# Optimization experiments

Measured on AMD Instinct MI355X. Metric: run time of the kernel, lower is better.

Reference implementation:

```python
import jax, jax.numpy as jnp
import numpy as np

N_NODES = 100000
N_EDGES = 3200000
N_GRAPHS = 2048
D_IN = 128
D_H = 128
D_OUT = 2
BN_EPS = 1e-5


def setup_inputs() -> dict:
    key = jax.random.key(0)
    ks = jax.random.split(key, 24)
    x = jax.random.normal(ks[0], (N_NODES, D_IN), dtype=jnp.float32)
    edge_index = jax.random.randint(ks[1], (2, N_EDGES), 0, N_NODES, dtype=jnp.int64)
    batch = jnp.sort(jax.random.randint(ks[2], (N_NODES,), 0, N_GRAPHS, dtype=jnp.int64))

    def lin(k, din, dout):
        return jax.random.normal(k, (din, dout), dtype=jnp.float32) / np.sqrt(din)

    inp = {
        'x': x, 'edge_index': edge_index, 'batch': batch,
        'W1': lin(ks[3], D_IN, D_H), 'b1': jnp.zeros((D_H,), jnp.float32),
        'W2': lin(ks[4], D_H, D_H), 'b2': jnp.zeros((D_H,), jnp.float32),
        'W3': lin(ks[5], D_H, D_H), 'b3': jnp.zeros((D_H,), jnp.float32),
    }
    for i, kk in zip((1, 2, 3), (ks[6], ks[7], ks[8])):
        inp[f'bn{i}_g'] = 1.0 + 0.1 * jax.random.normal(jax.random.fold_in(kk, 0), (D_H,), jnp.float32)
        inp[f'bn{i}_b'] = 0.1 * jax.random.normal(jax.random.fold_in(kk, 1), (D_H,), jnp.float32)
        inp[f'bn{i}_m'] = 0.1 * jax.random.normal(jax.random.fold_in(kk, 2), (D_H,), jnp.float32)
        inp[f'bn{i}_v'] = 0.5 + jax.random.uniform(jax.random.fold_in(kk, 3), (D_H,), jnp.float32)
    inp['fc1_W'] = lin(ks[9], D_H, D_H)
    inp['fc1_b'] = jnp.zeros((D_H,), jnp.float32)
    inp['fc2_W'] = lin(ks[10], D_H, D_OUT)
    inp['fc2_b'] = jnp.zeros((D_OUT,), jnp.float32)
    return inp


def _gcn_conv(x, W, b, src, dst, dinv):
    # h = X W, then out[dst] += (dinv[src]*dinv[dst]) * h[src]  (self-loops already in src/dst)
    h = x @ W
    norm = dinv[src] * dinv[dst]  # [E+N]
    msg = h[src] * norm[:, None]  # [E+N, D]
    out = jax.ops.segment_sum(msg, dst, num_segments=N_NODES)
    return out + b


def _bn_eval(x, g, b, m, v):
    return (x - m) * (g * jax.lax.rsqrt(v + BN_EPS)) + b


def reference(x, edge_index, batch, W1, b1, W2, b2, W3, b3,
              bn1_g, bn1_b, bn1_m, bn1_v, bn2_g, bn2_b, bn2_m, bn2_v,
              bn3_g, bn3_b, bn3_m, bn3_v, fc1_W, fc1_b, fc2_W, fc2_b):
    loops = jnp.arange(N_NODES, dtype=edge_index.dtype)
    src = jnp.concatenate([edge_index[0], loops])
    dst = jnp.concatenate([edge_index[1], loops])
    deg = jax.ops.segment_sum(jnp.ones_like(dst, dtype=x.dtype), dst, num_segments=N_NODES)
    dinv = jnp.where(deg > 0, jax.lax.rsqrt(jnp.maximum(deg, 1.0)), 0.0)

    h = jax.nn.relu(_bn_eval(_gcn_conv(x, W1, b1, src, dst, dinv), bn1_g, bn1_b, bn1_m, bn1_v))
    h = jax.nn.relu(_bn_eval(_gcn_conv(h, W2, b2, src, dst, dinv), bn2_g, bn2_b, bn2_m, bn2_v))
    h = jax.nn.relu(_bn_eval(_gcn_conv(h, W3, b3, src, dst, dinv), bn3_g, bn3_b, bn3_m, bn3_v))

    # global mean pool over graphs
    sums = jax.ops.segment_sum(h, batch, num_segments=N_GRAPHS)
    cnts = jax.ops.segment_sum(jnp.ones((N_NODES,), h.dtype), batch, num_segments=N_GRAPHS)
    pooled = sums / jnp.maximum(cnts, 1.0)[:, None]  # [G, D_H]

    z = jax.nn.relu(pooled @ fc1_W + fc1_b)
    logits = z @ fc2_W + fc2_b
    return jax.nn.log_softmax(logits, axis=1)
```

## Files before the change

kernel.cpp:

```cpp
#include <hip/hip_runtime.h>
#include <stdint.h>

#define NN 100000
#define NE 3200000
#define NG 2048
#define DH 128

#define NBUK 196
#define BSH 9
#define BMASK 511
#define BUKCAP 18200
#define EPT 16
#define EPW 4096

typedef __attribute__((ext_vector_type(8))) short v8s;
typedef __attribute__((ext_vector_type(4))) float v4f;
typedef __attribute__((ext_vector_type(2))) float f2;

__device__ __forceinline__ float bf2f(unsigned short u) {
  union { unsigned int i; float f; } v; v.i = ((unsigned int)u) << 16; return v.f;
}
__device__ __forceinline__ unsigned short f2bf(float f) {
  union { float f; unsigned int i; } v; v.f = f;
  unsigned int i = v.i;
  unsigned int r = (i + 0x7FFFu + ((i >> 16) & 1u)) >> 16;
  return (unsigned short)r;
}
__device__ __forceinline__ int eload(const void* p, long long i, int is64) {
  return is64 ? (int)((const long long*)p)[i] : ((const int*)p)[i];
}
__device__ __forceinline__ float pload(const void* p, int i, int isbf) {
  return isbf ? bf2f(((const unsigned short*)p)[i]) : ((const float*)p)[i];
}
__device__ __forceinline__ void upadd2(unsigned int w, f2& acc) {
  union { unsigned int u; float f; } a, b;
  a.u = w << 16; b.u = w & 0xffff0000u;
  f2 u; u.x = a.f; u.y = b.f;
  acc += u;
}

constexpr size_t al(size_t x) { return (x + 255) & ~size_t(255); }
constexpr size_t OFF_FLAGS = 0;
constexpr size_t OFF_DINV  = 256;
constexpr size_t OFF_ROWP  = al(OFF_DINV + 4ull * NN);
constexpr size_t OFF_GSTART= al(OFF_ROWP + 4ull * (NN + 1));
constexpr size_t OFF_BCUR  = al(OFF_GSTART + 4ull * (NG + 1));
constexpr size_t OFF_WT    = al(OFF_BCUR + 1024);
constexpr size_t OFF_FC1W  = al(OFF_WT + 2ull * 3 * 16384);
constexpr size_t OFF_FC2W  = al(OFF_FC1W + 4ull * 16384);
constexpr size_t OFF_PVEC  = al(OFF_FC2W + 4ull * 256);
constexpr size_t OFF_AC    = al(OFF_PVEC + 4ull * 17 * 128);
constexpr size_t OFF_COL   = al(OFF_AC + 4ull * 768);
constexpr size_t OFF_H     = al(OFF_COL + 4ull * NE);
constexpr size_t OFF_Y     = al(OFF_H + 2ull * NN * 128);
constexpr size_t WS_NEED   = OFF_Y + 2ull * NN * 128;
constexpr size_t OFF_REC   = OFF_H;


__global__ __launch_bounds__(256) void probe_k(const void* edge, const void* batch,
                                               const void* x, int* flags, int* bcur) {
  __shared__ int cnt_e, cnt_b, cnt_f;
  int t = threadIdx.x;
  bcur[t] = 0;
  if (t == 0) { cnt_e = 0; cnt_b = 0; cnt_f = 0; }
  __syncthreads();
  int le = 0, lb = 0, lf = 0;
  for (int i = t; i < 512; i += 256) {
    uint2 p = ((const uint2*)edge)[i + 64];
    if (p.y != 0) le++;
  }
  for (int i = t; i < 512; i += 256) {
    uint2 p = ((const uint2*)batch)[50000 - 512 + i];
    if (p.y != 0) lb++;
  }
  for (int i = t; i < 4096; i += 256) {
    unsigned short u = ((const unsigned short*)x)[i];
    int e = (u >> 7) & 0xFF;
    if (e >= 0x90) lf++;
  }
  atomicAdd(&cnt_e, le); atomicAdd(&cnt_b, lb); atomicAdd(&cnt_f, lf);
  __syncthreads();
  if (t == 0) {
    flags[0] = (cnt_e == 0);
    flags[1] = (cnt_b == 0);
    flags[2] = (cnt_f < 16);
    flags[3] = 1;
  }
}

struct Ptrs { const void* p[22]; };

__global__ __launch_bounds__(256) void norm_param_k(Ptrs ptrs, const int* flags,
    unsigned short* Wt, float* fc1W, float* fc2W, float* pvec) {
  int isbf = flags[2];
  int idx = blockIdx.x * 256 + threadIdx.x;
  if (idx < 3 * 16384) {
    int l = idx / 16384, rem = idx % 16384;
    int c = rem >> 7, k = rem & 127;
    const void* W = ptrs.p[2 * l];
    Wt[l * 16384 + c * DH + k] = f2bf(pload(W, k * DH + c, isbf));
  } else if (idx < 4 * 16384) {
    int jj = idx - 3 * 16384;
    fc1W[jj] = pload(ptrs.p[18], jj, isbf);
  } else if (idx < 4 * 16384 + 256) {
    int jj = idx - 4 * 16384;
    fc2W[jj] = pload(ptrs.p[20], jj, isbf);
  } else if (idx < 4 * 16384 + 256 + 17 * 128) {
    int jj = idx - (4 * 16384 + 256);
    int slot = jj >> 7, e = jj & 127;
    int pi = (slot < 3) ? (1 + 2 * slot) : (slot < 15) ? (slot + 3) : (slot == 15 ? 19 : 21);
    if (slot == 16 && e >= 2) return;
    pvec[slot * 128 + e] = pload(ptrs.p[pi], e, isbf);
  }
}

__global__ __launch_bounds__(256) void prep_k(const float* pvec, float* AC) {
  int idx = blockIdx.x * 256 + threadIdx.x;
  if (idx >= 384) return;
  int l = idx >> 7, d = idx & 127;
  float b  = pvec[l * 128 + d];
  float g  = pvec[(3 + 4 * l) * 128 + d];
  float bb = pvec[(4 + 4 * l) * 128 + d];
  float m  = pvec[(5 + 4 * l) * 128 + d];
  float v  = pvec[(6 + 4 * l) * 128 + d];
  float s = g * rsqrtf(v + 1e-5f);
  AC[l * 256 + d] = s;
  AC[l * 256 + 128 + d] = (b - m) * s + bb;
}

__global__ __launch_bounds__(256) void partition_k(const void* edge, const int* flags,
    int* bcur, unsigned long long* recs) {
  __shared__ int lhist[NBUK];
  __shared__ int lbase[NBUK];
  __shared__ int lrank[NBUK];
  int t = threadIdx.x;
  for (int b = t; b < NBUK; b += 256) { lhist[b] = 0; lrank[b] = 0; }
  __syncthreads();
  long long e0 = (long long)blockIdx.x * EPW;
  int f = flags[0];
  int sv[EPT], dv[EPT];
  #pragma unroll
  for (int k = 0; k < EPT; ++k) {
    long long e = e0 + k * 256 + t;
    int s = 0, d = -1;
    if (e < NE) {
      s = eload(edge, e, f);
      d = eload(edge, NE + e, f);
      if ((unsigned)s >= NN || (unsigned)d >= NN) d = -1;
    }
    sv[k] = s; dv[k] = d;
    if (d >= 0) atomicAdd(&lhist[d >> BSH], 1);
  }
  __syncthreads();
  for (int b = t; b < NBUK; b += 256)
    lbase[b] = atomicAdd(&bcur[b], lhist[b]);
  __syncthreads();
  #pragma unroll
  for (int k = 0; k < EPT; ++k) {
    int d = dv[k];
    if (d >= 0) {
      int b = d >> BSH;
      int r = atomicAdd(&lrank[b], 1);
      int pos = lbase[b] + r;
      if (pos < BUKCAP)
        recs[(size_t)b * BUKCAP + pos] =
            ((unsigned long long)(unsigned)d << 32) | (unsigned)sv[k];
    }
  }
}

__global__ __launch_bounds__(256) void csr_build_k(const unsigned long long* recs,
    const int* bcur, int* rowp, int* colv, float* dinv) {
  __shared__ int lh[512];
  __shared__ int lcur[512];
  __shared__ int lts[256];
  __shared__ int lstart;
  int b = blockIdx.x, t = threadIdx.x;
  {
    int v = (t < b && t < NBUK) ? min(bcur[t], BUKCAP) : 0;
    lts[t] = v; __syncthreads();
    for (int off = 128; off > 0; off >>= 1) {
      if (t < off) lts[t] += lts[t + off];
      __syncthreads();
    }
    if (t == 0) lstart = lts[0];
  }
  for (int i = t; i < 512; i += 256) lh[i] = 0;
  __syncthreads();
  int cnt = min(bcur[b], BUKCAP);
  const unsigned long long* rb = recs + (size_t)b * BUKCAP;
  for (int i = t; i < cnt; i += 256)
    atomicAdd(&lh[(int)(rb[i] >> 32) & BMASK], 1);
  __syncthreads();
  int e0 = lh[2 * t], e1 = lh[2 * t + 1];
  lts[t] = e0 + e1; __syncthreads();
  for (int off = 1; off < 256; off <<= 1) {
    int x = (t >= off) ? lts[t - off] : 0;
    __syncthreads();
    lts[t] += x;
    __syncthreads();
  }
  int pre = lts[t] - (e0 + e1);
  int base = b << BSH;
  int n0 = base + 2 * t, n1 = base + 2 * t + 1;
  int r0 = lstart + pre, r1 = lstart + pre + e0;
  if (n0 < NN) { rowp[n0] = r0; dinv[n0] = rsqrtf((float)(e0 + 1)); }
  if (n1 < NN) { rowp[n1] = r1; dinv[n1] = rsqrtf((float)(e1 + 1)); }
  lcur[2 * t] = r0; lcur[2 * t + 1] = r1;
  if (b == NBUK - 1 && t == 255) rowp[NN] = lstart + lts[255];
  __syncthreads();
  for (int i = t; i < cnt; i += 256) {
    unsigned long long rec = rb[i];
    int d = (int)(rec >> 32);
    int s = (int)(rec & 0xffffffffu);
    int p = atomicAdd(&lcur[d & BMASK], 1);
    colv[p] = s;
  }
}

__global__ __launch_bounds__(256) void gbound_k(const void* batch, const int* flags,
                                                int* gstart) {
  int i = blockIdx.x * 256 + threadIdx.x;
  if (i >= NN) return;
  int f = flags[1];
  int b = eload(batch, i, f);
  if ((unsigned)b >= NG) b = NG - 1;
  int bp = -1;
  if (i > 0) {
    bp = eload(batch, i - 1, f);
    if ((unsigned)bp >= NG) bp = NG - 1;
  }
  for (int g = bp + 1; g <= b; ++g) gstart[g] = i;
  if (i == NN - 1) {
    for (int g = b + 1; g <= NG; ++g) gstart[g] = NN;
  }
}

__global__ __launch_bounds__(256) void gemm_k(const void* A, const int* flagp,
    const unsigned short* Wt, const float* dinv, unsigned short* H) {
  const int wave = threadIdx.x >> 6;
  const int lane = threadIdx.x & 63;
  const int rowbase = blockIdx.x * 64 + wave * 16;
  const int r = lane & 15;
  const int g = lane >> 4;
  const int isb = flagp[0];
  int arow = rowbase + r;
  int arowc = (arow < NN) ? arow : 0;

  v8s a[4];
  if (isb) {
    const uint4* Ab = (const uint4*)A;
    #pragma unroll
    for (int ks = 0; ks < 4; ++ks) {
      union { uint4 u; v8s v; } t;
      t.u = Ab[(arowc * DH + ks * 32 + g * 8) >> 3];
      a[ks] = t.v;
    }
  } else {
    const float4* Af = (const float4*)A;
    #pragma unroll
    for (int ks = 0; ks < 4; ++ks) {
      int bi = (arowc * DH + ks * 32 + g * 8) >> 2;
      float4 f0 = Af[bi], f1 = Af[bi + 1];
      v8s t;
      t[0]=(short)f2bf(f0.x); t[1]=(short)f2bf(f0.y); t[2]=(short)f2bf(f0.z); t[3]=(short)f2bf(f0.w);
      t[4]=(short)f2bf(f1.x); t[5]=(short)f2bf(f1.y); t[6]=(short)f2bf(f1.z); t[7]=(short)f2bf(f1.w);
      a[ks] = t;
    }
  }
  int orow0 = rowbase + g * 4;
  float dv[4];
  #pragma unroll
  for (int j = 0; j < 4; ++j) {
    int orow = orow0 + j;
    dv[j] = dinv[(orow < NN) ? orow : 0];
  }
  const uint4* Wb = (const uint4*)Wt;
  #pragma unroll
  for (int ct = 0; ct < 8; ++ct) {
    v4f acc = {0.f, 0.f, 0.f, 0.f};
    #pragma unroll
    for (int ks = 0; ks < 4; ++ks) {
      union { uint4 u; v8s v; } t;
      t.u = Wb[((ct * 16 + r) * DH + ks * 32 + g * 8) >> 3];
      acc = __builtin_amdgcn_mfma_f32_16x16x32_bf16(a[ks], t.v, acc, 0, 0, 0);
    }
    #pragma unroll
    for (int j = 0; j < 4; ++j) {
      int orow = orow0 + j;
      if (orow < NN) H[orow * DH + ct * 16 + r] = f2bf(acc[j] * dv[j]);
    }
  }
}

__global__ __launch_bounds__(256) void agg_k(const unsigned short* H, const int* rowp,
    const int* colv, const float* dinv, const float* Avec, const float* Cvec,
    unsigned short* Y) {
  int n = blockIdx.x * 4 + (threadIdx.x >> 6);
  if (n >= NN) return;
  int lane = threadIdx.x & 63;
  int q = lane >> 4;
  int c16 = lane & 15;
  const uint4* Hc = (const uint4*)H + c16;
  f2 a01 = {0.f, 0.f}, a23 = {0.f, 0.f}, a45 = {0.f, 0.f}, a67 = {0.f, 0.f};
  int beg = rowp[n], end = rowp[n + 1];
  int j = beg;
  #define ACC4(v) do { upadd2((v).x, a01); upadd2((v).y, a23); \
                       upadd2((v).z, a45); upadd2((v).w, a67); } while (0)
  for (; j + 16 <= end; j += 16) {
    int s0 = colv[j + q];
    int s1 = colv[j + 4 + q];
    int s2 = colv[j + 8 + q];
    int s3 = colv[j + 12 + q];
    uint4 v0 = Hc[s0 * 16];
    uint4 v1 = Hc[s1 * 16];
    uint4 v2 = Hc[s2 * 16];
    uint4 v3 = Hc[s3 * 16];
    ACC4(v0); ACC4(v1); ACC4(v2); ACC4(v3);
  }
  for (; j + 4 <= end; j += 4) {
    int s0 = colv[j + q];
    uint4 v0 = Hc[s0 * 16];
    ACC4(v0);
  }
  if (j + q < end) {
    uint4 v0 = Hc[colv[j + q] * 16];
    ACC4(v0);
  }
  #undef ACC4
  #pragma unroll
  for (int m = 16; m <= 32; m <<= 1) {
    a01.x += __shfl_xor(a01.x, m); a01.y += __shfl_xor(a01.y, m);
    a23.x += __shfl_xor(a23.x, m); a23.y += __shfl_xor(a23.y, m);
    a45.x += __shfl_xor(a45.x, m); a45.y += __shfl_xor(a45.y, m);
    a67.x += __shfl_xor(a67.x, m); a67.y += __shfl_xor(a67.y, m);
  }
  if (q == 0) {
    uint4 sv = Hc[n * 16];
    upadd2(sv.x, a01); upadd2(sv.y, a23);
    upadd2(sv.z, a45); upadd2(sv.w, a67);
    float dvn = dinv[n];
    int f0 = c16 * 8;
    float y0 = fmaxf(a01.x * dvn * Avec[f0+0] + Cvec[f0+0], 0.f);
    float y1 = fmaxf(a01.y * dvn * Avec[f0+1] + Cvec[f0+1], 0.f);
    float y2 = fmaxf(a23.x * dvn * Avec[f0+2] + Cvec[f0+2], 0.f);
    float y3 = fmaxf(a23.y * dvn * Avec[f0+3] + Cvec[f0+3], 0.f);
    float y4 = fmaxf(a45.x * dvn * Avec[f0+4] + Cvec[f0+4], 0.f);
    float y5 = fmaxf(a45.y * dvn * Avec[f0+5] + Cvec[f0+5], 0.f);
    float y6 = fmaxf(a67.x * dvn * Avec[f0+6] + Cvec[f0+6], 0.f);
    float y7 = fmaxf(a67.y * dvn * Avec[f0+7] + Cvec[f0+7], 0.f);
    uint4 o;
    o.x = (unsigned int)f2bf(y0) | ((unsigned int)f2bf(y1) << 16);
    o.y = (unsigned int)f2bf(y2) | ((unsigned int)f2bf(y3) << 16);
    o.z = (unsigned int)f2bf(y4) | ((unsigned int)f2bf(y5) << 16);
    o.w = (unsigned int)f2bf(y6) | ((unsigned int)f2bf(y7) << 16);
    ((uint4*)Y)[n * 16 + c16] = o;
  }
}

__global__ __launch_bounds__(256) void pool_k(const unsigned short* Y, const int* gstart,
                                              float* pooled) {
  int g = blockIdx.x * 4 + (threadIdx.x >> 6);
  if (g >= NG) return;
  int lane = threadIdx.x & 63;
  const unsigned int* Yu = (const unsigned int*)Y;
  int beg = gstart[g], end = gstart[g + 1];
  int cnt = end - beg;
  float a0 = 0.f, a1 = 0.f;
  for (int i = beg; i < end; ++i) {
    unsigned int v = Yu[i * 64 + lane];
    a0 += bf2f((unsigned short)v); a1 += bf2f((unsigned short)(v >> 16));
  }
  float inv = 1.f / fmaxf((float)cnt, 1.f);
  pooled[g * DH + lane * 2]     = a0 * inv;
  pooled[g * DH + lane * 2 + 1] = a1 * inv;
}

__global__ __launch_bounds__(256) void fc1_k(const float* pooled, const float* fc1W,
                                             const float* pvec, float* Z) {
  int idx = blockIdx.x * 256 + threadIdx.x;
  int g = idx >> 7, c = idx & 127;
  if (g >= NG) return;
  float acc = 0.f;
  const float* pr = pooled + g * DH;
  #pragma unroll 8
  for (int k = 0; k < DH; ++k) acc += pr[k] * fc1W[k * DH + c];
  acc += pvec[15 * 128 + c];
  Z[g * DH + c] = fmaxf(acc, 0.f);
}

__global__ __launch_bounds__(256) void fc2_k(const float* Z, const float* fc2W,
                                             const float* pvec, float* out) {
  int g = blockIdx.x * 256 + threadIdx.x;
  if (g >= NG) return;
  float l0 = pvec[16 * 128 + 0], l1 = pvec[16 * 128 + 1];
  const float* zr = Z + g * DH;
  #pragma unroll 8
  for (int k = 0; k < DH; ++k) { float z = zr[k]; l0 += z * fc2W[k * 2]; l1 += z * fc2W[k * 2 + 1]; }
  float m = fmaxf(l0, l1);
  float lse = m + logf(expf(l0 - m) + expf(l1 - m));
  out[g * 2]     = l0 - lse;
  out[g * 2 + 1] = l1 - lse;
}

extern "C" void kernel_launch(void* const* d_in, const int* in_sizes, int n_in,
                              void* d_out, int out_size, void* d_ws, size_t ws_size,
                              hipStream_t stream) {
  char* ws = (char*)d_ws;
  int*   flags  = (int*)(ws + OFF_FLAGS);
  float* dinvp  = (float*)(ws + OFF_DINV);
  int*   rowp   = (int*)(ws + OFF_ROWP);
  int*   gstart = (int*)(ws + OFF_GSTART);
  int*   bcur   = (int*)(ws + OFF_BCUR);
  unsigned short* Wt  = (unsigned short*)(ws + OFF_WT);
  float* fc1W   = (float*)(ws + OFF_FC1W);
  float* fc2W   = (float*)(ws + OFF_FC2W);
  float* pvec   = (float*)(ws + OFF_PVEC);
  float* AC     = (float*)(ws + OFF_AC);
  int*   colv   = (int*)(ws + OFF_COL);
  unsigned short* Hbuf = (unsigned short*)(ws + OFF_H);
  unsigned short* Ybuf = (unsigned short*)(ws + OFF_Y);
  unsigned long long* recs = (unsigned long long*)(ws + OFF_REC);
  float* pooled = (float*)(ws + OFF_COL);
  float* Z      = (float*)(ws + OFF_COL + 4ull * NG * DH);

  const void* x     = d_in[0];
  const void* edge  = d_in[1];
  const void* batch = d_in[2];

  probe_k<<<1, 256, 0, stream>>>(edge, batch, x, flags, bcur);

  Ptrs P;
  for (int i = 0; i < 22; ++i) P.p[i] = d_in[3 + i];
  norm_param_k<<<266, 256, 0, stream>>>(P, flags, Wt, fc1W, fc2W, pvec);
  prep_k<<<2, 256, 0, stream>>>(pvec, AC);

  partition_k<<<(NE + EPW - 1) / EPW, 256, 0, stream>>>(edge, flags, bcur, recs);
  gbound_k<<<(NN + 255) / 256, 256, 0, stream>>>(batch, flags, gstart);
  csr_build_k<<<NBUK, 256, 0, stream>>>(recs, bcur, rowp, colv, dinvp);

  const int GB = (NN + 63) / 64;
  gemm_k<<<GB, 256, 0, stream>>>(x, flags + 2, Wt, dinvp, Hbuf);
  agg_k<<<NN / 4, 256, 0, stream>>>(Hbuf, rowp, colv, dinvp, AC, AC + 128, Ybuf);
  gemm_k<<<GB, 256, 0, stream>>>(Ybuf, flags + 3, Wt + 16384, dinvp, Hbuf);
  agg_k<<<NN / 4, 256, 0, stream>>>(Hbuf, rowp, colv, dinvp, AC + 256, AC + 384, Ybuf);
  gemm_k<<<GB, 256, 0, stream>>>(Ybuf, flags + 3, Wt + 32768, dinvp, Hbuf);
  agg_k<<<NN / 4, 256, 0, stream>>>(Hbuf, rowp, colv, dinvp, AC + 512, AC + 640, Ybuf);

  pool_k<<<NG / 4, 256, 0, stream>>>(Ybuf, gstart, pooled);
  fc1_k<<<(NG * DH) / 256, 256, 0, stream>>>(pooled, fc1W, pvec, Z);
  fc2_k<<<(NG + 255) / 256, 256, 0, stream>>>(Z, fc2W, pvec, (float*)d_out);
}
```

Baseline: 564.6 us.

## Fuse aggregation with next-layer GEMM via LDS staging

Adds a kernel that aggregates 64 node rows per block, applies the BN and ReLU epilogue, stages the bf16 result in shared memory, and then runs the next layer's MFMA GEMM on it. The intermediate Y is no longer written to and read back from global memory between layers 1-2 and 2-3, and two launches are removed. The gather loop is also deepened to 32 edges per iteration. The trade-off is less parallelism: each wave now handles 16 rows in sequence instead of one row per wave, with only 1563 blocks, which can hurt latency hiding for the irregular gathers.

Measured after the change: 609.7 us. +8.0%, slower.

```diff
diff --git a/kernel.cpp b/kernel.cpp
--- a/kernel.cpp
+++ b/kernel.cpp
@@ -13,6 +13,8 @@
 #define EPT 16
 #define EPW 4096
 
+#define LROW 136
+
 typedef __attribute__((ext_vector_type(8))) short v8s;
 typedef __attribute__((ext_vector_type(4))) float v4f;
 typedef __attribute__((ext_vector_type(2))) float f2;
@@ -37,6 +39,40 @@
   a.u = w << 16; b.u = w & 0xffff0000u;
   f2 u; u.x = a.f; u.y = b.f;
   acc += u;
+}
+#define ACC4(v) do { upadd2((v).x, a01); upadd2((v).y, a23); \
+                     upadd2((v).z, a45); upadd2((v).w, a67); } while (0)
+
+__device__ __forceinline__ void gather_row(const uint4* Hc, const int* colv,
+    int beg, int end, int q, f2& a01, f2& a23, f2& a45, f2& a67) {
+  int j = beg;
+  for (; j + 32 <= end; j += 32) {
+    int s0 = colv[j + q],      s1 = colv[j + 4 + q];
+    int s2 = colv[j + 8 + q],  s3 = colv[j + 12 + q];
+    int s4 = colv[j + 16 + q], s5 = colv[j + 20 + q];
+    int s6 = colv[j + 24 + q], s7 = colv[j + 28 + q];
+    uint4 v0 = Hc[s0 * 16]; uint4 v1 = Hc[s1 * 16];
+    uint4 v2 = Hc[s2 * 16]; uint4 v3 = Hc[s3 * 16];
+    uint4 v4 = Hc[s4 * 16]; uint4 v5 = Hc[s5 * 16];
+    uint4 v6 = Hc[s6 * 16]; uint4 v7 = Hc[s7 * 16];
+    ACC4(v0); ACC4(v1); ACC4(v2); ACC4(v3);
+    ACC4(v4); ACC4(v5); ACC4(v6); ACC4(v7);
+  }
+  for (; j + 16 <= end; j += 16) {
+    int s0 = colv[j + q],     s1 = colv[j + 4 + q];
+    int s2 = colv[j + 8 + q], s3 = colv[j + 12 + q];
+    uint4 v0 = Hc[s0 * 16]; uint4 v1 = Hc[s1 * 16];
+    uint4 v2 = Hc[s2 * 16]; uint4 v3 = Hc[s3 * 16];
+    ACC4(v0); ACC4(v1); ACC4(v2); ACC4(v3);
+  }
+  for (; j + 4 <= end; j += 4) {
+    uint4 v0 = Hc[colv[j + q] * 16];
+    ACC4(v0);
+  }
+  if (j + q < end) {
+    uint4 v0 = Hc[colv[j + q] * 16];
+    ACC4(v0);
+  }
 }
 
 constexpr size_t al(size_t x) { return (x + 255) & ~size_t(255); }
@@ -293,6 +329,89 @@
   }
 }
 
+__global__ __launch_bounds__(256) void aggemm_k(const unsigned short* H,
+    const int* rowp, const int* colv, const float* dinv,
+    const float* Avec, const float* Cvec, const unsigned short* Wt,
+    unsigned short* Hout) {
+  __shared__ unsigned short Ylds[64 * LROW];
+  int wid = threadIdx.x >> 6, lane = threadIdx.x & 63;
+  int q = lane >> 4, c16 = lane & 15;
+  int base = blockIdx.x * 64;
+  const uint4* Hc = (const uint4*)H + c16;
+  for (int i = 0; i < 16; ++i) {
+    int row = wid * 16 + i;
+    int n = base + row;
+    if (n < NN) {
+      f2 a01 = {0.f,0.f}, a23 = {0.f,0.f}, a45 = {0.f,0.f}, a67 = {0.f,0.f};
+      int beg = rowp[n], end = rowp[n + 1];
+      gather_row(Hc, colv, beg, end, q, a01, a23, a45, a67);
+      #pragma unroll
+      for (int m = 16; m <= 32; m <<= 1) {
+        a01.x += __shfl_xor(a01.x, m); a01.y += __shfl_xor(a01.y, m);
+        a23.x += __shfl_xor(a23.x, m); a23.y += __shfl_xor(a23.y, m);
+        a45.x += __shfl_xor(a45.x, m); a45.y += __shfl_xor(a45.y, m);
+        a67.x += __shfl_xor(a67.x, m); a67.y += __shfl_xor(a67.y, m);
+      }
+      if (q == 0) {
+        uint4 sv = Hc[n * 16];
+        upadd2(sv.x, a01); upadd2(sv.y, a23);
+        upadd2(sv.z, a45); upadd2(sv.w, a67);
+        float dvn = dinv[n];
+        int f0 = c16 * 8;
+        float y0 = fmaxf(a01.x * dvn * Avec[f0+0] + Cvec[f0+0], 0.f);
+        float y1 = fmaxf(a01.y * dvn * Avec[f0+1] + Cvec[f0+1], 0.f);
+        float y2 = fmaxf(a23.x * dvn * Avec[f0+2] + Cvec[f0+2], 0.f);
+        float y3 = fmaxf(a23.y * dvn * Avec[f0+3] + Cvec[f0+3], 0.f);
+        float y4 = fmaxf(a45.x * dvn * Avec[f0+4] + Cvec[f0+4], 0.f);
+        float y5 = fmaxf(a45.y * dvn * Avec[f0+5] + Cvec[f0+5], 0.f);
+        float y6 = fmaxf(a67.x * dvn * Avec[f0+6] + Cvec[f0+6], 0.f);
+        float y7 = fmaxf(a67.y * dvn * Avec[f0+7] + Cvec[f0+7], 0.f);
+        uint4 o;
+        o.x = (unsigned int)f2bf(y0) | ((unsigned int)f2bf(y1) << 16);
+        o.y = (unsigned int)f2bf(y2) | ((unsigned int)f2bf(y3) << 16);
+        o.z = (unsigned int)f2bf(y4) | ((unsigned int)f2bf(y5) << 16);
+        o.w = (unsigned int)f2bf(y6) | ((unsigned int)f2bf(y7) << 16);
+        *(uint4*)&Ylds[row * LROW + c16 * 8] = o;
+      }
+    } else if (q == 0) {
+      uint4 z = {0u, 0u, 0u, 0u};
+      *(uint4*)&Ylds[row * LROW + c16 * 8] = z;
+    }
+  }
+  __syncthreads();
+  int r = lane & 15, g = lane >> 4;
+  v8s a[4];
+  #pragma unroll
+  for (int ks = 0; ks < 4; ++ks) {
+    union { uint4 u; v8s v; } t;
+    t.u = *(const uint4*)&Ylds[(wid * 16 + r) * LROW + ks * 32 + g * 8];
+    a[ks] = t.v;
+  }
+  int orow0 = base + wid * 16 + g * 4;
+  float dv[4];
+  #pragma unroll
+  for (int j = 0; j < 4; ++j) {
+    int orow = orow0 + j;
+    dv[j] = dinv[(orow < NN) ? orow : 0];
+  }
+  const uint4* Wb = (const uint4*)Wt;
+  #pragma unroll
+  for (int ct = 0; ct < 8; ++ct) {
+    v4f acc = {0.f, 0.f, 0.f, 0.f};
+    #pragma unroll
+    for (int ks = 0; ks < 4; ++ks) {
+      union { uint4 u; v8s v; } t;
+      t.u = Wb[((ct * 16 + r) * DH + ks * 32 + g * 8) >> 3];
+      acc = __builtin_amdgcn_mfma_f32_16x16x32_bf16(a[ks], t.v, acc, 0, 0, 0);
+    }
+    #pragma unroll
+    for (int j = 0; j < 4; ++j) {
+      int orow = orow0 + j;
+      if (orow < NN) Hout[orow * DH + ct * 16 + r] = f2bf(acc[j] * dv[j]);
+    }
+  }
+}
+
 __global__ __launch_bounds__(256) void agg_k(const unsigned short* H, const int* rowp,
     const int* colv, const float* dinv, const float* Avec, const float* Cvec,
     unsigned short* Y) {
@@ -302,32 +421,8 @@
   int q = lane >> 4;
   int c16 = lane & 15;
   const uint4* Hc = (const uint4*)H + c16;
-  f2 a01 = {0.f, 0.f}, a23 = {0.f, 0.f}, a45 = {0.f, 0.f}, a67 = {0.f, 0.f};
-  int beg = rowp[n], end = rowp[n + 1];
-  int j = beg;
-  #define ACC4(v) do { upadd2((v).x, a01); upadd2((v).y, a23); \
-                       upadd2((v).z, a45); upadd2((v).w, a67); } while (0)
-  for (; j + 16 <= end; j += 16) {
-    int s0 = colv[j + q];
-    int s1 = colv[j + 4 + q];
-    int s2 = colv[j + 8 + q];
-    int s3 = colv[j + 12 + q];
-    uint4 v0 = Hc[s0 * 16];
-    uint4 v1 = Hc[s1 * 16];
-    uint4 v2 = Hc[s2 * 16];
-    uint4 v3 = Hc[s3 * 16];
-    ACC4(v0); ACC4(v1); ACC4(v2); ACC4(v3);
-  }
-  for (; j + 4 <= end; j += 4) {
-    int s0 = colv[j + q];
-    uint4 v0 = Hc[s0 * 16];
-    ACC4(v0);
-  }
-  if (j + q < end) {
-    uint4 v0 = Hc[colv[j + q] * 16];
-    ACC4(v0);
-  }
-  #undef ACC4
+  f2 a01 = {0.f,0.f}, a23 = {0.f,0.f}, a45 = {0.f,0.f}, a67 = {0.f,0.f};
+  gather_row(Hc, colv, rowp[n], rowp[n + 1], q, a01, a23, a45, a67);
   #pragma unroll
   for (int m = 16; m <= 32; m <<= 1) {
     a01.x += __shfl_xor(a01.x, m); a01.y += __shfl_xor(a01.y, m);
@@ -441,10 +536,10 @@
 
   const int GB = (NN + 63) / 64;
   gemm_k<<<GB, 256, 0, stream>>>(x, flags + 2, Wt, dinvp, Hbuf);
-  agg_k<<<NN / 4, 256, 0, stream>>>(Hbuf, rowp, colv, dinvp, AC, AC + 128, Ybuf);
-  gemm_k<<<GB, 256, 0, stream>>>(Ybuf, flags + 3, Wt + 16384, dinvp, Hbuf);
-  agg_k<<<NN / 4, 256, 0, stream>>>(Hbuf, rowp, colv, dinvp, AC + 256, AC + 384, Ybuf);
-  gemm_k<<<GB, 256, 0, stream>>>(Ybuf, flags + 3, Wt + 32768, dinvp, Hbuf);
+  aggemm_k<<<GB, 256, 0, stream>>>(Hbuf, rowp, colv, dinvp, AC, AC + 128,
+                                   Wt + 16384, Ybuf);
+  aggemm_k<<<GB, 256, 0, stream>>>(Ybuf, rowp, colv, dinvp, AC + 256, AC + 384,
+                                   Wt + 32768, Hbuf);
   agg_k<<<NN / 4, 256, 0, stream>>>(Hbuf, rowp, colv, dinvp, AC + 512, AC + 640, Ybuf);
 
   pool_k<<<NG / 4, 256, 0, stream>>>(Ybuf, gstart, pooled);
```
